# Kernel optimization log

Hardware: AMD Instinct MI355X
Metric: run time of the kernel (lower is better)

Reference implementation:

```python
import jax, jax.numpy as jnp
from jax import lax
import numpy as np

SQRT2 = float(np.sqrt(2.0))


def _linear(x, W, b):
    # torch Linear convention: W is (out, in)
    return x @ W.T + b


def _causal_cnn_glu(x, w, b):
    # x: (B, T, C). Causal pad k-1=4 on time, Conv1d C->2C k=5, GLU, residual.
    xp = jnp.pad(x, ((0, 0), (4, 0), (0, 0)))
    y = lax.conv_general_dilated(
        xp.transpose(0, 2, 1), w, window_strides=(1,), padding='VALID',
        dimension_numbers=('NCH', 'OIH', 'NCH'))
    y = y + b[None, :, None]
    y = y.transpose(0, 2, 1)  # (B, T, 2C)
    a, g = jnp.split(y, 2, axis=-1)
    return (a * jax.nn.sigmoid(g) + x) / SQRT2


def setup_inputs() -> dict:
    key = jax.random.key(0)
    ks = jax.random.split(key, 12)
    B, T_enc, T_dec, D, IN = 32, 1024, 2048, 256, 80
    s_d = 1.0 / np.sqrt(D)
    s_in = 1.0 / np.sqrt(IN)
    return {
        'encoder_outputs': jax.random.normal(ks[0], (B, T_enc, D), jnp.float32),
        'first_embedding': jax.random.normal(ks[1], (B, T_enc, D), jnp.float32),
        'mel_inputs': jax.random.uniform(ks[2], (B, T_dec, IN), jnp.float32),
        'W_lin': jax.random.normal(ks[3], (D, IN), jnp.float32) * s_in,
        'b_lin': jnp.zeros((D,), jnp.float32),
        'conv_w0': jax.random.normal(ks[4], (2 * D, D, 5), jnp.float32) * s_d,
        'conv_b0': jnp.zeros((2 * D,), jnp.float32),
        'conv_w1': jax.random.normal(ks[5], (2 * D, D, 5), jnp.float32) * s_d,
        'conv_b1': jnp.zeros((2 * D,), jnp.float32),
        'W_attn': jax.random.normal(ks[6], (D, D), jnp.float32) * s_d,
        'b_attn': jnp.zeros((D,), jnp.float32),
        'W_proj': jax.random.normal(ks[7], (IN, D), jnp.float32) * s_d,
        'b_proj': jnp.zeros((IN,), jnp.float32),
    }


def reference(encoder_outputs, first_embedding, mel_inputs,
              W_lin, b_lin, conv_w0, conv_b0, conv_w1, conv_b1,
              W_attn, b_attn, W_proj, b_proj):
    B, T_dec, _ = mel_inputs.shape
    D = encoder_outputs.shape[-1]
    x = _linear(mel_inputs, W_lin, b_lin)                    # (B, T_dec, 256)
    # prepend zero initial input, drop last frame (shift right)
    x = jnp.concatenate([jnp.zeros((B, 1, D), x.dtype), x], axis=1)[:, :-1, :]
    h = _causal_cnn_glu(x, conv_w0, conv_b0)                 # CNN layer 0
    q = _linear(h, W_attn, b_attn)                           # attention after layer 0
    scores = jnp.einsum('btd,bsd->bts', q, encoder_outputs)  # (B, T_dec, T_enc)
    attn = jax.nn.softmax(scores, axis=-1)
    c = jnp.einsum('bts,bsd->btd', attn, encoder_outputs + first_embedding)
    h = h + c
    h = _causal_cnn_glu(h, conv_w1, conv_b1)                 # CNN layer 1 (no attention)
    return _linear(h, W_proj, b_proj)                        # (B, T_dec, in_dim)
```

## Files before the change

### kernel.cpp

```cpp
#include <hip/hip_runtime.h>
#include <math.h>

#define BB 32
#define TD 2048
#define TE 1024
#define DIM 256
#define INDIM 80

typedef __attribute__((ext_vector_type(8))) _Float16 f16x8;
typedef __attribute__((ext_vector_type(4))) float f32x4;

__device__ __forceinline__ float sigmoidf_(float x){ return 1.f/(1.f+__expf(-x)); }

__global__ __launch_bounds__(256) void k_wprep(const float* __restrict__ w,
    _Float16* __restrict__ Wf)
{
  int i = blockIdx.x*256 + threadIdx.x;
  int o = i / 1280;
  int kk = i - o*1280;
  int tap = kk >> 8, ic = kk & 255;
  Wf[i] = (_Float16)w[(size_t)o*1280 + ic*5 + tap];
}

__global__ __launch_bounds__(256) void k_qwprep(const float* __restrict__ W,
    _Float16* __restrict__ Wh, _Float16* __restrict__ Wl)
{
  int i = blockIdx.x*256 + threadIdx.x;
  float f = W[i];
  _Float16 h = (_Float16)f;
  Wh[i] = h;
  Wl[i] = (_Float16)(f - (float)h);
}

__global__ __launch_bounds__(256) void k_lwprep(const float* __restrict__ W,
    _Float16* __restrict__ Wh, _Float16* __restrict__ Wl)
{
  int i = blockIdx.x*256 + threadIdx.x;
  int d = i / 96, k = i - d*96;
  float f = (k < INDIM) ? W[d*INDIM + k] : 0.f;
  _Float16 h = (_Float16)f;
  Wh[i] = h;
  Wl[i] = (_Float16)(f - (float)h);
}

__global__ __launch_bounds__(256) void k_pwprep(const float* __restrict__ W,
    _Float16* __restrict__ Wh, _Float16* __restrict__ Wl)
{
  int i = blockIdx.x*256 + threadIdx.x;
  float f = W[i];
  _Float16 h = (_Float16)f;
  Wh[i] = h;
  Wl[i] = (_Float16)(f - (float)h);
}

__global__ __launch_bounds__(256) void k_eprep(const float* __restrict__ enc,
    const float* __restrict__ emb, _Float16* __restrict__ Eh,
    _Float16* __restrict__ EVt)
{
  __shared__ float ls[64][65];
  int blk = blockIdx.x;
  int dt = blk & 3, st = (blk>>2) & 15, b = blk >> 6;
  int s0 = st*64, d0 = dt*64;
  int tid = threadIdx.x;
  for (int k=0;k<16;k++){
    int idx = k*256 + tid;
    int r = idx >> 6, c = idx & 63;
    size_t gi = ((size_t)b*TE + s0 + r)*DIM + d0 + c;
    float e = enc[gi];
    ls[r][c] = e + emb[gi];
    Eh[gi] = (_Float16)e;
  }
  __syncthreads();
  for (int k=0;k<16;k++){
    int idx = k*256 + tid;
    int r = idx >> 6, c = idx & 63;
    EVt[((size_t)b*DIM + d0 + r)*TE + s0 + c] = (_Float16)ls[c][r];
  }
}

__global__ __launch_bounds__(256) void k_lin_mfma(const float* __restrict__ mel,
    const _Float16* __restrict__ Wh, const _Float16* __restrict__ Wl,
    const float* __restrict__ bias, _Float16* __restrict__ X)
{
  __shared__ __align__(16) _Float16 ms[64*104];
  int blk = blockIdx.x;
  int b = blk >> 5;
  int t0 = (blk & 31) << 6;
  int tid = threadIdx.x;

  for (int i = tid; i < 64*12; i += 256){
    int row = i / 12, cg = (i - row*12) * 8;
    int t = t0 + row - 1;
    f16x8 v = {};
    if (t >= 0 && cg < INDIM){
      const float4* p = (const float4*)(mel + ((size_t)b*TD + t)*INDIM + cg);
      float4 f0 = p[0], f1 = p[1];
      v[0]=(_Float16)f0.x; v[1]=(_Float16)f0.y; v[2]=(_Float16)f0.z; v[3]=(_Float16)f0.w;
      v[4]=(_Float16)f1.x; v[5]=(_Float16)f1.y; v[6]=(_Float16)f1.z; v[7]=(_Float16)f1.w;
    }
    *(f16x8*)&ms[row*104 + cg] = v;
  }
  __syncthreads();

  int wave = tid >> 6, lane = tid & 63;
  int l15 = lane & 15, l4 = lane >> 4;
  int mb = wave << 4;

  f16x8 am[3];
  #pragma unroll
  for (int kc=0;kc<3;kc++) am[kc] = *(f16x8*)&ms[(mb + l15)*104 + kc*32 + l4*8];

  for (int dt=0; dt<16; dt++){
    size_t wrow = (size_t)(dt*16 + l15)*96 + l4*8;
    f32x4 a = (f32x4){0.f,0.f,0.f,0.f};
    #pragma unroll
    for (int kc=0;kc<3;kc++){
      f16x8 bh = *(const f16x8*)(Wh + wrow + kc*32);
      f16x8 bl = *(const f16x8*)(Wl + wrow + kc*32);
      a = __builtin_amdgcn_mfma_f32_16x16x32_f16(am[kc], bh, a, 0,0,0);
      a = __builtin_amdgcn_mfma_f32_16x16x32_f16(am[kc], bl, a, 0,0,0);
    }
    int d = dt*16 + l15;
    float bv = bias[d];
    #pragma unroll
    for (int r=0;r<4;r++){
      int m = mb + l4*4 + r;
      int t = t0 + m;
      X[((size_t)b*TD + t)*DIM + d] = (t==0) ? (_Float16)0.f : (_Float16)(a[r] + bv);
    }
  }
}

template<int TIN_F32, int TOUT_F32>
__global__ __launch_bounds__(256) void k_conv_mfma(const void* __restrict__ Xin_,
    const _Float16* __restrict__ Wf, const float* __restrict__ bias,
    void* __restrict__ Hout_)
{
  __shared__ __align__(16) _Float16 as[68*264];
  int id = blockIdx.x;
  int dtile = id & 3, mtile = id >> 2;
  int b = mtile >> 5;
  int t0 = (mtile & 31) << 6;
  int d0 = dtile << 6;
  int tid = threadIdx.x;

  for (int i = tid; i < 68*32; i += 256){
    int row = i >> 5, cg = (i & 31) << 3;
    int t = t0 - 4 + row;
    f16x8 v = {};
    if (t >= 0){
      if (TIN_F32){
        const float4* p = (const float4*)((const float*)Xin_ + ((size_t)b*TD + t)*DIM + cg);
        float4 f0 = p[0], f1 = p[1];
        v[0]=(_Float16)f0.x; v[1]=(_Float16)f0.y; v[2]=(_Float16)f0.z; v[3]=(_Float16)f0.w;
        v[4]=(_Float16)f1.x; v[5]=(_Float16)f1.y; v[6]=(_Float16)f1.z; v[7]=(_Float16)f1.w;
      } else {
        v = *(const f16x8*)((const _Float16*)Xin_ + ((size_t)b*TD + t)*DIM + cg);
      }
    }
    *(f16x8*)&as[row*264 + cg] = v;
  }
  __syncthreads();

  int lane = tid & 63, wave = tid >> 6;
  int l15 = lane & 15, l4 = lane >> 4;
  int dA = d0 + (wave << 4) + l15;

  const _Float16* pA = Wf + (size_t)dA*1280 + l4*8;
  const _Float16* pG = Wf + (size_t)(256 + dA)*1280 + l4*8;

  f32x4 aca[4], acg[4];
  #pragma unroll
  for (int mt=0;mt<4;mt++){ aca[mt]=(f32x4){0.f,0.f,0.f,0.f}; acg[mt]=(f32x4){0.f,0.f,0.f,0.f}; }

  f16x8 bA = *(const f16x8*)pA;
  f16x8 bG = *(const f16x8*)pG;
  #pragma unroll
  for (int kc = 0; kc < 40; ++kc){
    f16x8 nA = bA, nG = bG;
    if (kc < 39){
      nA = *(const f16x8*)(pA + (kc+1)*32);
      nG = *(const f16x8*)(pG + (kc+1)*32);
    }
    int tap = kc >> 3;
    int ic0 = (kc & 7) << 5;
    int abase = (l15 + tap)*264 + ic0 + l4*8;
    #pragma unroll
    for (int mt=0;mt<4;mt++){
      f16x8 av = *(f16x8*)&as[abase + mt*16*264];
      aca[mt] = __builtin_amdgcn_mfma_f32_16x16x32_f16(av, bA, aca[mt], 0,0,0);
      acg[mt] = __builtin_amdgcn_mfma_f32_16x16x32_f16(av, bG, acg[mt], 0,0,0);
    }
    bA = nA; bG = nG;
  }

  const float is2 = 0.7071067811865476f;
  float ba = bias[dA], bg = bias[256 + dA];
  #pragma unroll
  for (int mt=0; mt<4; mt++){
    #pragma unroll
    for (int r=0;r<4;r++){
      int m = mt*16 + l4*4 + r;
      size_t orow = ((size_t)b*TD + t0 + m)*DIM;
      float xr = TIN_F32 ? ((const float*)Xin_)[orow + dA]
                         : (float)as[(m+4)*264 + dA];
      float a = aca[mt][r] + ba;
      float g = acg[mt][r] + bg;
      float o = (a*sigmoidf_(g) + xr)*is2;
      if (TOUT_F32) ((float*)Hout_)[orow + dA] = o;
      else          ((_Float16*)Hout_)[orow + dA] = (_Float16)o;
    }
  }
}

__global__ __launch_bounds__(256) void k_attn(float* __restrict__ H,
    const _Float16* __restrict__ Wqh, const _Float16* __restrict__ Wql,
    const float* __restrict__ bq,
    const _Float16* __restrict__ Eh, const _Float16* __restrict__ EVt)
{
  __shared__ __align__(16) _Float16 ech[64*264];
  __shared__ __align__(16) _Float16 evch[256*72];
  __shared__ __align__(16) _Float16 pbuf[4][16][72];

  int i = blockIdx.x;
  int b = (i & 7) | ((i >> 8) << 3);
  int t0 = ((i >> 3) & 31) << 6;
  int tid = threadIdx.x;
  int wave = tid >> 6, lane = tid & 63;
  int l15 = lane & 15, l4 = lane >> 4;
  int mb = wave << 4;

  f16x8 ah[8];
  {
    const float* hrow = H + ((size_t)b*TD + t0 + mb + l15)*DIM;
    #pragma unroll
    for (int kc=0;kc<8;kc++){
      const float4* p = (const float4*)(hrow + kc*32 + l4*8);
      float4 f0 = p[0], f1 = p[1];
      f16x8 v;
      v[0]=(_Float16)f0.x; v[1]=(_Float16)f0.y; v[2]=(_Float16)f0.z; v[3]=(_Float16)f0.w;
      v[4]=(_Float16)f1.x; v[5]=(_Float16)f1.y; v[6]=(_Float16)f1.z; v[7]=(_Float16)f1.w;
      ah[kc] = v;
    }
  }

  f32x4 qacc[16];
  for (int ot=0;ot<16;ot++){
    size_t wrow = (size_t)(ot*16 + l15)*256 + l4*8;
    f32x4 a = (f32x4){0.f,0.f,0.f,0.f};
    #pragma unroll
    for (int kc=0;kc<8;kc++){
      f16x8 bh = *(const f16x8*)(Wqh + wrow + kc*32);
      f16x8 bl = *(const f16x8*)(Wql + wrow + kc*32);
      a = __builtin_amdgcn_mfma_f32_16x16x32_f16(ah[kc], bh, a, 0,0,0);
      a = __builtin_amdgcn_mfma_f32_16x16x32_f16(ah[kc], bl, a, 0,0,0);
    }
    qacc[ot] = a;
  }
  #pragma unroll
  for (int ot=0;ot<16;ot++){
    float bqv = bq[ot*16 + l15];
    #pragma unroll
    for (int r=0;r<4;r++) qacc[ot][r] += bqv;
  }

  #pragma unroll
  for (int ot=0;ot<16;ot++){
    int o = ot*16 + l15;
    #pragma unroll
    for (int r=0;r<4;r++)
      ech[(mb + l4*4 + r)*264 + o] = (_Float16)qacc[ot][r];
  }
  f16x8 aqh[8];
  #pragma unroll
  for (int kc=0;kc<8;kc++) aqh[kc] = *(f16x8*)&ech[(mb + l15)*264 + kc*32 + l4*8];
  #pragma unroll
  for (int ot=0;ot<16;ot++){
    int o = ot*16 + l15;
    #pragma unroll
    for (int r=0;r<4;r++){
      float v = qacc[ot][r];
      _Float16 h = (_Float16)v;
      ech[(mb + l4*4 + r)*264 + o] = (_Float16)(v - (float)h);
    }
  }
  f16x8 aql[8];
  #pragma unroll
  for (int kc=0;kc<8;kc++) aql[kc] = *(f16x8*)&ech[(mb + l15)*264 + kc*32 + l4*8];

  f32x4 oacc[16];
  #pragma unroll
  for (int dt=0;dt<16;dt++) oacc[dt] = (f32x4){0.f,0.f,0.f,0.f};
  float mrun[4], lrun[4];
  #pragma unroll
  for (int r=0;r<4;r++){ mrun[r] = -3.0e38f; lrun[r] = 0.f; }

  const _Float16* Ehb = Eh + (size_t)b*TE*DIM;
  const _Float16* EVb = EVt + (size_t)b*DIM*TE;

  for (int s0 = 0; s0 < TE; s0 += 64){
    __syncthreads();
    #pragma unroll
    for (int it=0; it<8; it++){
      int slot = it*256 + tid;
      int row = slot >> 5, cg = (slot & 31) << 3;
      *(f16x8*)&ech[row*264 + cg] = *(const f16x8*)(Ehb + (size_t)(s0+row)*DIM + cg);
    }
    #pragma unroll
    for (int it=0; it<8; it++){
      int slot = it*256 + tid;
      int row = slot >> 3, cg = (slot & 7) << 3;
      *(f16x8*)&evch[row*72 + cg] = *(const f16x8*)(EVb + (size_t)row*TE + s0 + cg);
    }
    __syncthreads();

    f32x4 sacc[4];
    #pragma unroll
    for (int st=0;st<4;st++){
      int er = (st*16 + l15)*264 + l4*8;
      f32x4 a = (f32x4){0.f,0.f,0.f,0.f};
      #pragma unroll
      for (int kc=0;kc<8;kc++){
        f16x8 bh = *(f16x8*)&ech[er + kc*32];
        a = __builtin_amdgcn_mfma_f32_16x16x32_f16(aqh[kc], bh, a, 0,0,0);
        a = __builtin_amdgcn_mfma_f32_16x16x32_f16(aql[kc], bh, a, 0,0,0);
      }
      sacc[st] = a;
    }
    float alpha[4];
    #pragma unroll
    for (int r=0;r<4;r++){
      float cm = fmaxf(fmaxf(sacc[0][r], sacc[1][r]), fmaxf(sacc[2][r], sacc[3][r]));
      cm = fmaxf(cm, __shfl_xor(cm, 1));
      cm = fmaxf(cm, __shfl_xor(cm, 2));
      cm = fmaxf(cm, __shfl_xor(cm, 4));
      cm = fmaxf(cm, __shfl_xor(cm, 8));
      float mnew = fmaxf(mrun[r], cm);
      alpha[r] = __expf(mrun[r] - mnew);
      mrun[r] = mnew;
      float ps = 0.f;
      #pragma unroll
      for (int st=0;st<4;st++){
        float p = __expf(sacc[st][r] - mnew);
        sacc[st][r] = p;
        ps += p;
      }
      ps += __shfl_xor(ps, 1);
      ps += __shfl_xor(ps, 2);
      ps += __shfl_xor(ps, 4);
      ps += __shfl_xor(ps, 8);
      lrun[r] = lrun[r]*alpha[r] + ps;
    }
    #pragma unroll
    for (int dt=0;dt<16;dt++){
      #pragma unroll
      for (int r=0;r<4;r++) oacc[dt][r] *= alpha[r];
    }
    #pragma unroll
    for (int st=0;st<4;st++){
      #pragma unroll
      for (int r=0;r<4;r++)
        pbuf[wave][l4*4+r][st*16+l15] = (_Float16)sacc[st][r];
    }
    #pragma unroll
    for (int kp=0;kp<2;kp++){
      f16x8 ap = *(f16x8*)&pbuf[wave][l15][kp*32 + l4*8];
      #pragma unroll
      for (int dt=0;dt<16;dt++){
        f16x8 bv = *(f16x8*)&evch[(dt*16 + l15)*72 + kp*32 + l4*8];
        oacc[dt] = __builtin_amdgcn_mfma_f32_16x16x32_f16(ap, bv, oacc[dt], 0,0,0);
      }
    }
  }

  float linv[4];
  #pragma unroll
  for (int r=0;r<4;r++) linv[r] = 1.f / lrun[r];
  #pragma unroll
  for (int dt=0;dt<16;dt++){
    int d = dt*16 + l15;
    #pragma unroll
    for (int r=0;r<4;r++){
      int t = t0 + mb + l4*4 + r;
      float* hp = &H[((size_t)b*TD + t)*DIM + d];
      *hp += oacc[dt][r] * linv[r];
    }
  }
}

__global__ __launch_bounds__(256) void k_proj_mfma(const _Float16* __restrict__ Hin,
    const _Float16* __restrict__ Wh, const _Float16* __restrict__ Wl,
    const float* __restrict__ bias, float* __restrict__ out)
{
  int blk = blockIdx.x;
  int b = blk >> 5;
  int t0 = (blk & 31) << 6;
  int tid = threadIdx.x;
  int wave = tid >> 6, lane = tid & 63;
  int l15 = lane & 15, l4 = lane >> 4;
  int mb = wave << 4;

  f16x8 ah[8];
  const _Float16* hrow = Hin + ((size_t)b*TD + t0 + mb + l15)*DIM;
  #pragma unroll
  for (int kc=0;kc<8;kc++) ah[kc] = *(const f16x8*)(hrow + kc*32 + l4*8);

  #pragma unroll
  for (int nt=0; nt<5; nt++){
    size_t wrow = (size_t)(nt*16 + l15)*256 + l4*8;
    f32x4 a = (f32x4){0.f,0.f,0.f,0.f};
    #pragma unroll
    for (int kc=0;kc<8;kc++){
      f16x8 bh = *(const f16x8*)(Wh + wrow + kc*32);
      f16x8 bl = *(const f16x8*)(Wl + wrow + kc*32);
      a = __builtin_amdgcn_mfma_f32_16x16x32_f16(ah[kc], bh, a, 0,0,0);
      a = __builtin_amdgcn_mfma_f32_16x16x32_f16(ah[kc], bl, a, 0,0,0);
    }
    int n = nt*16 + l15;
    float bv = bias[n];
    #pragma unroll
    for (int r=0;r<4;r++){
      int t = t0 + mb + l4*4 + r;
      out[((size_t)b*TD + t)*INDIM + n] = a[r] + bv;
    }
  }
}

extern "C" void kernel_launch(void* const* d_in, const int* in_sizes, int n_in,
                              void* d_out, int out_size, void* d_ws, size_t ws_size,
                              hipStream_t stream) {
  const float* enc   = (const float*)d_in[0];
  const float* emb   = (const float*)d_in[1];
  const float* mel   = (const float*)d_in[2];
  const float* W_lin = (const float*)d_in[3];
  const float* b_lin = (const float*)d_in[4];
  const float* w0    = (const float*)d_in[5];
  const float* b0    = (const float*)d_in[6];
  const float* w1    = (const float*)d_in[7];
  const float* b1    = (const float*)d_in[8];
  const float* Wq    = (const float*)d_in[9];
  const float* bq    = (const float*)d_in[10];
  const float* Wp    = (const float*)d_in[11];
  const float* bp    = (const float*)d_in[12];
  float* out = (float*)d_out;

  const size_t NTOK = (size_t)BB*TD*DIM;
  const size_t NE   = (size_t)BB*TE*DIM;
  _Float16* Xb  = (_Float16*)d_ws;
  float*    H   = (float*)(Xb + NTOK);
  _Float16* Wf0 = (_Float16*)(H + NTOK);
  _Float16* Wf1 = Wf0 + (size_t)512*1280;
  _Float16* Wqh = Wf1 + (size_t)512*1280;
  _Float16* Wql = Wqh + 65536;
  _Float16* Wlh = Wql + 65536;
  _Float16* Wll = Wlh + 24576;
  _Float16* Wph = Wll + 24576;
  _Float16* Wpl = Wph + 20480;
  _Float16* Eh  = Xb;
  _Float16* EVt = Xb + NE;
  _Float16* Pb  = Xb;

  k_wprep    <<<2560, 256, 0, stream>>>(w0, Wf0);
  k_wprep    <<<2560, 256, 0, stream>>>(w1, Wf1);
  k_qwprep   <<<256,  256, 0, stream>>>(Wq, Wqh, Wql);
  k_lwprep   <<<96,   256, 0, stream>>>(W_lin, Wlh, Wll);
  k_pwprep   <<<80,   256, 0, stream>>>(Wp, Wph, Wpl);
  k_lin_mfma <<<1024, 256, 0, stream>>>(mel, Wlh, Wll, b_lin, Xb);
  k_conv_mfma<0,1><<<4096, 256, 0, stream>>>(Xb, Wf0, b0, H);
  k_eprep    <<<2048, 256, 0, stream>>>(enc, emb, Eh, EVt);
  k_attn     <<<1024, 256, 0, stream>>>(H, Wqh, Wql, bq, Eh, EVt);
  k_conv_mfma<1,0><<<4096, 256, 0, stream>>>(H, Wf1, b1, Pb);
  k_proj_mfma<<<1024, 256, 0, stream>>>(Pb, Wph, Wpl, bp, out);
}
```

Measured before the change: 897.2 us.

## Double-buffer K tiles via async global-to-LDS loads and split PV by D columns

The attention kernel now stages encoder K tiles into a double-buffered, XOR-swizzled LDS buffer with global_load_lds, prefetching the next tile while computing the current one. The PV product is repartitioned so each wave owns 64 output columns for all 64 query rows, reading V directly from global into registers. Probabilities and rescale factors are shared across waves through LDS. This removes the per-iteration LDS staging of V and hides K load latency. The cost is an extra barrier per tile and uncoalesced, uncached-in-LDS V reads from global memory.

```diff
diff --git a/kernel.cpp b/kernel.cpp
--- a/kernel.cpp
+++ b/kernel.cpp
@@ -11,6 +11,12 @@
 typedef __attribute__((ext_vector_type(4))) float f32x4;
 
 __device__ __forceinline__ float sigmoidf_(float x){ return 1.f/(1.f+__expf(-x)); }
+
+__device__ __forceinline__ void cp16(const _Float16* g, _Float16* l){
+  __builtin_amdgcn_global_load_lds(
+      (const __attribute__((address_space(1))) unsigned int*)g,
+      (__attribute__((address_space(3))) unsigned int*)l, 16, 0, 0);
+}
 
 __global__ __launch_bounds__(256) void k_wprep(const float* __restrict__ w,
     _Float16* __restrict__ Wf)
@@ -213,14 +219,27 @@
   }
 }
 
+__device__ __forceinline__ void stage_k(const _Float16* __restrict__ Ehb,
+    _Float16* __restrict__ dst, int srow0, int wave, int lane)
+{
+  int r2 = lane >> 5, cu = lane & 31;
+  #pragma unroll
+  for (int ii=0; ii<8; ii++){
+    int row = (ii*4 + wave)*2 + r2;
+    cp16(Ehb + (size_t)(srow0 + row)*DIM + ((cu ^ (row & 7)) << 3),
+         dst + (ii*4 + wave)*512);
+  }
+}
+
 __global__ __launch_bounds__(256) void k_attn(float* __restrict__ H,
     const _Float16* __restrict__ Wqh, const _Float16* __restrict__ Wql,
     const float* __restrict__ bq,
     const _Float16* __restrict__ Eh, const _Float16* __restrict__ EVt)
 {
-  __shared__ __align__(16) _Float16 ech[64*264];
-  __shared__ __align__(16) _Float16 evch[256*72];
-  __shared__ __align__(16) _Float16 pbuf[4][16][72];
+  __shared__ __align__(16) _Float16 Kb[2][64*256];
+  __shared__ __align__(16) _Float16 pb[64][72];
+  __shared__ float alphas[64];
+  __shared__ float linvs[64];
 
   int i = blockIdx.x;
   int b = (i & 7) | ((i >> 8) << 3);
@@ -230,6 +249,11 @@
   int l15 = lane & 15, l4 = lane >> 4;
   int mb = wave << 4;
 
+  const _Float16* Ehb = Eh + (size_t)b*TE*DIM;
+  const _Float16* EVb = EVt + (size_t)b*DIM*TE;
+
+  stage_k(Ehb, &Kb[0][0], 0, wave, lane);
+
   f16x8 ah[8];
   {
     const float* hrow = H + ((size_t)b*TD + t0 + mb + l15)*DIM;
@@ -269,11 +293,13 @@
     int o = ot*16 + l15;
     #pragma unroll
     for (int r=0;r<4;r++)
-      ech[(mb + l4*4 + r)*264 + o] = (_Float16)qacc[ot][r];
-  }
+      Kb[1][(mb + l4*4 + r)*256 + o] = (_Float16)qacc[ot][r];
+  }
+  __syncthreads();
   f16x8 aqh[8];
   #pragma unroll
-  for (int kc=0;kc<8;kc++) aqh[kc] = *(f16x8*)&ech[(mb + l15)*264 + kc*32 + l4*8];
+  for (int kc=0;kc<8;kc++) aqh[kc] = *(f16x8*)&Kb[1][(mb + l15)*256 + kc*32 + l4*8];
+  __syncthreads();
   #pragma unroll
   for (int ot=0;ot<16;ot++){
     int o = ot*16 + l15;
@@ -281,52 +307,53 @@
     for (int r=0;r<4;r++){
       float v = qacc[ot][r];
       _Float16 h = (_Float16)v;
-      ech[(mb + l4*4 + r)*264 + o] = (_Float16)(v - (float)h);
-    }
-  }
+      Kb[1][(mb + l4*4 + r)*256 + o] = (_Float16)(v - (float)h);
+    }
+  }
+  __syncthreads();
   f16x8 aql[8];
   #pragma unroll
-  for (int kc=0;kc<8;kc++) aql[kc] = *(f16x8*)&ech[(mb + l15)*264 + kc*32 + l4*8];
-
-  f32x4 oacc[16];
-  #pragma unroll
-  for (int dt=0;dt<16;dt++) oacc[dt] = (f32x4){0.f,0.f,0.f,0.f};
+  for (int kc=0;kc<8;kc++) aql[kc] = *(f16x8*)&Kb[1][(mb + l15)*256 + kc*32 + l4*8];
+  __syncthreads();
+
+  f32x4 oacc[4][4];
+  #pragma unroll
+  for (int mt=0;mt<4;mt++)
+    #pragma unroll
+    for (int dt=0;dt<4;dt++) oacc[mt][dt] = (f32x4){0.f,0.f,0.f,0.f};
   float mrun[4], lrun[4];
   #pragma unroll
   for (int r=0;r<4;r++){ mrun[r] = -3.0e38f; lrun[r] = 0.f; }
-
-  const _Float16* Ehb = Eh + (size_t)b*TE*DIM;
-  const _Float16* EVb = EVt + (size_t)b*DIM*TE;
-
-  for (int s0 = 0; s0 < TE; s0 += 64){
-    __syncthreads();
-    #pragma unroll
-    for (int it=0; it<8; it++){
-      int slot = it*256 + tid;
-      int row = slot >> 5, cg = (slot & 31) << 3;
-      *(f16x8*)&ech[row*264 + cg] = *(const f16x8*)(Ehb + (size_t)(s0+row)*DIM + cg);
-    }
-    #pragma unroll
-    for (int it=0; it<8; it++){
-      int slot = it*256 + tid;
-      int row = slot >> 3, cg = (slot & 7) << 3;
-      *(f16x8*)&evch[row*72 + cg] = *(const f16x8*)(EVb + (size_t)row*TE + s0 + cg);
-    }
-    __syncthreads();
+  int dq = wave << 6;
+  int sw = l15 & 7;
+
+  #pragma unroll 2
+  for (int c = 0; c < 16; ++c){
+    int cur = c & 1;
+    int s0 = c << 6;
+    if (c < 15) stage_k(Ehb, &Kb[cur^1][0], s0 + 64, wave, lane);
 
     f32x4 sacc[4];
     #pragma unroll
     for (int st=0;st<4;st++){
-      int er = (st*16 + l15)*264 + l4*8;
+      const _Float16* kb = &Kb[cur][(st*16 + l15)*256];
       f32x4 a = (f32x4){0.f,0.f,0.f,0.f};
       #pragma unroll
       for (int kc=0;kc<8;kc++){
-        f16x8 bh = *(f16x8*)&ech[er + kc*32];
+        f16x8 bh = *(const f16x8*)(kb + (((kc*4 + l4) ^ sw) << 3));
         a = __builtin_amdgcn_mfma_f32_16x16x32_f16(aqh[kc], bh, a, 0,0,0);
         a = __builtin_amdgcn_mfma_f32_16x16x32_f16(aql[kc], bh, a, 0,0,0);
       }
       sacc[st] = a;
     }
+
+    f16x8 vv[2][4];
+    #pragma unroll
+    for (int kp=0;kp<2;kp++)
+      #pragma unroll
+      for (int dt=0;dt<4;dt++)
+        vv[kp][dt] = *(const f16x8*)(EVb + (size_t)(dq + dt*16 + l15)*TE + s0 + kp*32 + l4*8);
+
     float alpha[4];
     #pragma unroll
     for (int r=0;r<4;r++){
@@ -351,39 +378,58 @@
       ps += __shfl_xor(ps, 8);
       lrun[r] = lrun[r]*alpha[r] + ps;
     }
-    #pragma unroll
-    for (int dt=0;dt<16;dt++){
-      #pragma unroll
-      for (int r=0;r<4;r++) oacc[dt][r] *= alpha[r];
-    }
-    #pragma unroll
-    for (int st=0;st<4;st++){
+
+    #pragma unroll
+    for (int st=0;st<4;st++)
       #pragma unroll
       for (int r=0;r<4;r++)
-        pbuf[wave][l4*4+r][st*16+l15] = (_Float16)sacc[st][r];
+        pb[mb + l4*4 + r][st*16 + l15] = (_Float16)sacc[st][r];
+    if (l15 == 0){
+      #pragma unroll
+      for (int r=0;r<4;r++) alphas[mb + l4*4 + r] = alpha[r];
+    }
+    asm volatile("s_waitcnt lgkmcnt(0)" ::: "memory");
+    __builtin_amdgcn_s_barrier();
+
+    #pragma unroll
+    for (int mt=0;mt<4;mt++){
+      #pragma unroll
+      for (int r=0;r<4;r++){
+        float av = alphas[mt*16 + l4*4 + r];
+        #pragma unroll
+        for (int dt=0;dt<4;dt++) oacc[mt][dt][r] *= av;
+      }
     }
     #pragma unroll
     for (int kp=0;kp<2;kp++){
-      f16x8 ap = *(f16x8*)&pbuf[wave][l15][kp*32 + l4*8];
-      #pragma unroll
-      for (int dt=0;dt<16;dt++){
-        f16x8 bv = *(f16x8*)&evch[(dt*16 + l15)*72 + kp*32 + l4*8];
-        oacc[dt] = __builtin_amdgcn_mfma_f32_16x16x32_f16(ap, bv, oacc[dt], 0,0,0);
+      f16x8 pa[4];
+      #pragma unroll
+      for (int mt=0;mt<4;mt++) pa[mt] = *(f16x8*)&pb[mt*16 + l15][kp*32 + l4*8];
+      #pragma unroll
+      for (int dt=0;dt<4;dt++){
+        #pragma unroll
+        for (int mt=0;mt<4;mt++)
+          oacc[mt][dt] = __builtin_amdgcn_mfma_f32_16x16x32_f16(pa[mt], vv[kp][dt], oacc[mt][dt], 0,0,0);
       }
     }
-  }
-
-  float linv[4];
-  #pragma unroll
-  for (int r=0;r<4;r++) linv[r] = 1.f / lrun[r];
-  #pragma unroll
-  for (int dt=0;dt<16;dt++){
-    int d = dt*16 + l15;
+    __syncthreads();
+  }
+
+  if (l15 == 0){
+    #pragma unroll
+    for (int r=0;r<4;r++) linvs[mb + l4*4 + r] = 1.f / lrun[r];
+  }
+  __syncthreads();
+  #pragma unroll
+  for (int mt=0;mt<4;mt++){
     #pragma unroll
     for (int r=0;r<4;r++){
-      int t = t0 + mb + l4*4 + r;
-      float* hp = &H[((size_t)b*TD + t)*DIM + d];
-      *hp += oacc[dt][r] * linv[r];
+      float li = linvs[mt*16 + l4*4 + r];
+      int t = t0 + mt*16 + l4*4 + r;
+      float* hp = &H[((size_t)b*TD + t)*DIM + dq];
+      #pragma unroll
+      for (int dt=0;dt<4;dt++)
+        hp[dt*16 + l15] += oacc[mt][dt][r] * li;
     }
   }
 }
```

Result: faster. 868.8 us (-3.2%).

## Transpose attention MFMAs and stream K/V directly from global memory

Applied to the files above, without the earlier changes.

Rewrites the flash-attention inner loop so the score MFMAs use K as the A operand and Q as B. This makes each lane own a single query row, which turns the softmax max/sum into two cross-lane shuffles instead of four per row. The shared-memory K/V staging and the per-tile __syncthreads are removed: K and V fragments are read straight from global (L2) memory, and P is rearranged with register shuffles instead of an LDS buffer. It also adds a swizzled Q transpose buffer, skips the oacc rescale when no lane's max changed, and vectorizes the final residual add to float4. The cost is redundant global loads of K/V by the four waves with no LDS reuse, plus more exposed load latency without barriers to batch it.

```diff
diff --git a/kernel.cpp b/kernel.cpp
--- a/kernel.cpp
+++ b/kernel.cpp
@@ -11,6 +11,12 @@
 typedef __attribute__((ext_vector_type(4))) float f32x4;
 
 __device__ __forceinline__ float sigmoidf_(float x){ return 1.f/(1.f+__expf(-x)); }
+
+__device__ __forceinline__ unsigned pack2h(float a, float b){
+  union { _Float16 h[2]; unsigned u; } x;
+  x.h[0] = (_Float16)a; x.h[1] = (_Float16)b;
+  return x.u;
+}
 
 __global__ __launch_bounds__(256) void k_wprep(const float* __restrict__ w,
     _Float16* __restrict__ Wf)
@@ -218,9 +224,7 @@
     const float* __restrict__ bq,
     const _Float16* __restrict__ Eh, const _Float16* __restrict__ EVt)
 {
-  __shared__ __align__(16) _Float16 ech[64*264];
-  __shared__ __align__(16) _Float16 evch[256*72];
-  __shared__ __align__(16) _Float16 pbuf[4][16][72];
+  __shared__ __align__(16) _Float16 Qt[64*256];
 
   int i = blockIdx.x;
   int b = (i & 7) | ((i >> 8) << 3);
@@ -230,6 +234,9 @@
   int l15 = lane & 15, l4 = lane >> 4;
   int mb = wave << 4;
 
+  const _Float16* Ehb = Eh + (size_t)b*TE*DIM;
+  const _Float16* EVb = EVt + (size_t)b*DIM*TE;
+
   f16x8 ah[8];
   {
     const float* hrow = H + ((size_t)b*TD + t0 + mb + l15)*DIM;
@@ -268,123 +275,125 @@
   for (int ot=0;ot<16;ot++){
     int o = ot*16 + l15;
     #pragma unroll
-    for (int r=0;r<4;r++)
-      ech[(mb + l4*4 + r)*264 + o] = (_Float16)qacc[ot][r];
+    for (int r=0;r<4;r++){
+      int row = mb + l4*4 + r;
+      Qt[row*256 + (o ^ ((row & 7) << 3))] = (_Float16)qacc[ot][r];
+    }
   }
   f16x8 aqh[8];
-  #pragma unroll
-  for (int kc=0;kc<8;kc++) aqh[kc] = *(f16x8*)&ech[(mb + l15)*264 + kc*32 + l4*8];
+  {
+    int row = mb + l15, sw8 = l15 & 7;
+    #pragma unroll
+    for (int kc=0;kc<8;kc++)
+      aqh[kc] = *(f16x8*)&Qt[row*256 + (((kc*4 + l4) ^ sw8) << 3)];
+  }
   #pragma unroll
   for (int ot=0;ot<16;ot++){
     int o = ot*16 + l15;
     #pragma unroll
     for (int r=0;r<4;r++){
+      int row = mb + l4*4 + r;
       float v = qacc[ot][r];
       _Float16 h = (_Float16)v;
-      ech[(mb + l4*4 + r)*264 + o] = (_Float16)(v - (float)h);
+      Qt[row*256 + (o ^ ((row & 7) << 3))] = (_Float16)(v - (float)h);
     }
   }
   f16x8 aql[8];
-  #pragma unroll
-  for (int kc=0;kc<8;kc++) aql[kc] = *(f16x8*)&ech[(mb + l15)*264 + kc*32 + l4*8];
+  {
+    int row = mb + l15, sw8 = l15 & 7;
+    #pragma unroll
+    for (int kc=0;kc<8;kc++)
+      aql[kc] = *(f16x8*)&Qt[row*256 + (((kc*4 + l4) ^ sw8) << 3)];
+  }
 
   f32x4 oacc[16];
   #pragma unroll
   for (int dt=0;dt<16;dt++) oacc[dt] = (f32x4){0.f,0.f,0.f,0.f};
-  float mrun[4], lrun[4];
-  #pragma unroll
-  for (int r=0;r<4;r++){ mrun[r] = -3.0e38f; lrun[r] = 0.f; }
-
-  const _Float16* Ehb = Eh + (size_t)b*TE*DIM;
-  const _Float16* EVb = EVt + (size_t)b*DIM*TE;
-
-  for (int s0 = 0; s0 < TE; s0 += 64){
-    __syncthreads();
-    #pragma unroll
-    for (int it=0; it<8; it++){
-      int slot = it*256 + tid;
-      int row = slot >> 5, cg = (slot & 31) << 3;
-      *(f16x8*)&ech[row*264 + cg] = *(const f16x8*)(Ehb + (size_t)(s0+row)*DIM + cg);
-    }
-    #pragma unroll
-    for (int it=0; it<8; it++){
-      int slot = it*256 + tid;
-      int row = slot >> 3, cg = (slot & 7) << 3;
-      *(f16x8*)&evch[row*72 + cg] = *(const f16x8*)(EVb + (size_t)row*TE + s0 + cg);
-    }
-    __syncthreads();
+  float mrun = -3.0e38f, lrun = 0.f;
+
+  for (int c = 0; c < 16; ++c){
+    int s0 = c << 6;
 
     f32x4 sacc[4];
     #pragma unroll
     for (int st=0;st<4;st++){
-      int er = (st*16 + l15)*264 + l4*8;
+      const _Float16* kr = Ehb + (size_t)(s0 + st*16 + l15)*DIM + l4*8;
       f32x4 a = (f32x4){0.f,0.f,0.f,0.f};
       #pragma unroll
       for (int kc=0;kc<8;kc++){
-        f16x8 bh = *(f16x8*)&ech[er + kc*32];
-        a = __builtin_amdgcn_mfma_f32_16x16x32_f16(aqh[kc], bh, a, 0,0,0);
-        a = __builtin_amdgcn_mfma_f32_16x16x32_f16(aql[kc], bh, a, 0,0,0);
+        f16x8 kf = *(const f16x8*)(kr + kc*32);
+        a = __builtin_amdgcn_mfma_f32_16x16x32_f16(kf, aqh[kc], a, 0,0,0);
+        a = __builtin_amdgcn_mfma_f32_16x16x32_f16(kf, aql[kc], a, 0,0,0);
       }
       sacc[st] = a;
     }
-    float alpha[4];
-    #pragma unroll
-    for (int r=0;r<4;r++){
-      float cm = fmaxf(fmaxf(sacc[0][r], sacc[1][r]), fmaxf(sacc[2][r], sacc[3][r]));
-      cm = fmaxf(cm, __shfl_xor(cm, 1));
-      cm = fmaxf(cm, __shfl_xor(cm, 2));
-      cm = fmaxf(cm, __shfl_xor(cm, 4));
-      cm = fmaxf(cm, __shfl_xor(cm, 8));
-      float mnew = fmaxf(mrun[r], cm);
-      alpha[r] = __expf(mrun[r] - mnew);
-      mrun[r] = mnew;
-      float ps = 0.f;
+
+    float cm = sacc[0][0];
+    #pragma unroll
+    for (int st=0;st<4;st++)
       #pragma unroll
-      for (int st=0;st<4;st++){
+      for (int r=0;r<4;r++) cm = fmaxf(cm, sacc[st][r]);
+    cm = fmaxf(cm, __shfl_xor(cm, 16));
+    cm = fmaxf(cm, __shfl_xor(cm, 32));
+    float mnew = fmaxf(mrun, cm);
+    float alpha = __expf(mrun - mnew);
+    mrun = mnew;
+    float ps[4][4];
+    float lp = 0.f;
+    #pragma unroll
+    for (int st=0;st<4;st++)
+      #pragma unroll
+      for (int r=0;r<4;r++){
         float p = __expf(sacc[st][r] - mnew);
-        sacc[st][r] = p;
-        ps += p;
+        ps[st][r] = p;
+        lp += p;
       }
-      ps += __shfl_xor(ps, 1);
-      ps += __shfl_xor(ps, 2);
-      ps += __shfl_xor(ps, 4);
-      ps += __shfl_xor(ps, 8);
-      lrun[r] = lrun[r]*alpha[r] + ps;
+    lrun = lrun*alpha + lp;
+
+    unsigned pk[8];
+    #pragma unroll
+    for (int st=0;st<4;st++){
+      pk[st*2+0] = pack2h(ps[st][0], ps[st][1]);
+      pk[st*2+1] = pack2h(ps[st][2], ps[st][3]);
+    }
+    union { f16x8 v; unsigned u[4]; } pu[2];
+    #pragma unroll
+    for (int kp=0;kp<2;kp++)
+      #pragma unroll
+      for (int u=0;u<4;u++){
+        int srcl = l15 + (((l4*2 + (u>>1)) & 3) << 4);
+        unsigned gA = (unsigned)__shfl((int)pk[kp*4 + (u&1)], srcl);
+        unsigned gB = (unsigned)__shfl((int)pk[kp*4 + 2 + (u&1)], srcl);
+        pu[kp].u[u] = (l4 & 2) ? gB : gA;
+      }
+
+    if (__any(alpha != 1.0f)){
+      #pragma unroll
+      for (int dt=0;dt<16;dt++) oacc[dt] *= alpha;
     }
     #pragma unroll
     for (int dt=0;dt<16;dt++){
-      #pragma unroll
-      for (int r=0;r<4;r++) oacc[dt][r] *= alpha[r];
-    }
-    #pragma unroll
-    for (int st=0;st<4;st++){
-      #pragma unroll
-      for (int r=0;r<4;r++)
-        pbuf[wave][l4*4+r][st*16+l15] = (_Float16)sacc[st][r];
-    }
-    #pragma unroll
-    for (int kp=0;kp<2;kp++){
-      f16x8 ap = *(f16x8*)&pbuf[wave][l15][kp*32 + l4*8];
-      #pragma unroll
-      for (int dt=0;dt<16;dt++){
-        f16x8 bv = *(f16x8*)&evch[(dt*16 + l15)*72 + kp*32 + l4*8];
-        oacc[dt] = __builtin_amdgcn_mfma_f32_16x16x32_f16(ap, bv, oacc[dt], 0,0,0);
-      }
-    }
-  }
-
-  float linv[4];
-  #pragma unroll
-  for (int r=0;r<4;r++) linv[r] = 1.f / lrun[r];
+      const _Float16* vr = EVb + (size_t)(dt*16 + l15)*TE + s0 + l4*8;
+      f16x8 v0 = *(const f16x8*)(vr);
+      f16x8 v1 = *(const f16x8*)(vr + 32);
+      oacc[dt] = __builtin_amdgcn_mfma_f32_16x16x32_f16(v0, pu[0].v, oacc[dt], 0,0,0);
+      oacc[dt] = __builtin_amdgcn_mfma_f32_16x16x32_f16(v1, pu[1].v, oacc[dt], 0,0,0);
+    }
+  }
+
+  lrun += __shfl_xor(lrun, 16);
+  lrun += __shfl_xor(lrun, 32);
+  float linv = 1.f / lrun;
+  float* hp = &H[((size_t)b*TD + t0 + mb + l15)*DIM];
   #pragma unroll
   for (int dt=0;dt<16;dt++){
-    int d = dt*16 + l15;
-    #pragma unroll
-    for (int r=0;r<4;r++){
-      int t = t0 + mb + l4*4 + r;
-      float* hp = &H[((size_t)b*TD + t)*DIM + d];
-      *hp += oacc[dt][r] * linv[r];
-    }
+    float4* p = (float4*)&hp[dt*16 + l4*4];
+    float4 v = *p;
+    v.x += oacc[dt][0]*linv;
+    v.y += oacc[dt][1]*linv;
+    v.z += oacc[dt][2]*linv;
+    v.w += oacc[dt][3]*linv;
+    *p = v;
   }
 }
 
```

New measurement: 1.152 ms. +28.5%, slower.
